# Kernel optimization log

Hardware: AMD Instinct MI355X
Metric: run time of the kernel (lower is better)

## Reference

```python
import jax, jax.numpy as jnp
import numpy as np

N = 50000      # nodes
E = 500000     # edges
D_IN, D_HID, D_OUT = 128, 128, 64


def setup_inputs() -> dict:
    key = jax.random.key(0)
    ks = jax.random.split(key, 9)
    x = jax.random.normal(ks[0], (N, D_IN), dtype=jnp.float32)
    edge_index = jax.random.randint(ks[1], (2, E), 0, N, dtype=jnp.int64)
    s1 = 1.0 / np.sqrt(D_IN)
    s2 = 1.0 / np.sqrt(D_HID)
    W1 = jax.random.normal(ks[2], (D_IN, D_HID), dtype=jnp.float32) * s1
    b1 = jnp.zeros((D_HID,), dtype=jnp.float32)
    W2 = jax.random.normal(ks[3], (D_HID, D_HID), dtype=jnp.float32) * s2
    b2 = jnp.zeros((D_HID,), dtype=jnp.float32)
    W3 = jax.random.normal(ks[4], (D_HID, D_OUT), dtype=jnp.float32) * s2
    b3 = jnp.zeros((D_OUT,), dtype=jnp.float32)
    return {"x": x, "edge_index": edge_index,
            "W1": W1, "b1": b1, "W2": W2, "b2": b2, "W3": W3, "b3": b3}


def _gcn_norm(edge_index, num_nodes):
    # PyG GCNConv default: add self loops, symmetric normalization.
    loop = jnp.arange(num_nodes, dtype=edge_index.dtype)
    src = jnp.concatenate([edge_index[0], loop])  # [E+N]
    dst = jnp.concatenate([edge_index[1], loop])
    deg = jax.ops.segment_sum(jnp.ones_like(dst, dtype=jnp.float32), dst,
                              num_segments=num_nodes)
    dinv = jnp.where(deg > 0, jax.lax.rsqrt(deg), 0.0)
    norm = dinv[src] * dinv[dst]  # [E+N]
    return src, dst, norm


def _gcn_conv(x, W, b, src, dst, norm, num_nodes):
    # linear transform then degree-normalized scatter-add aggregation
    h = x @ W                                 # [N, F_out]
    msg = h[src] * norm[:, None]              # gather + scale  [E+N, F_out]
    out = jax.ops.segment_sum(msg, dst, num_segments=num_nodes)
    return out + b


def reference(x, edge_index, W1, b1, W2, b2, W3, b3):
    src, dst, norm = _gcn_norm(edge_index, N)
    h = _gcn_conv(x, W1, b1, src, dst, norm, N)
    h = _gcn_conv(h, W2, b2, src, dst, norm, N)
    h = _gcn_conv(h, W3, b3, src, dst, norm, N)
    return h
```

## Files before the change

kernel.cpp:

```cpp
#include <hip/hip_runtime.h>

#define DIN 128
#define DHID 128
#define DOUT 64

__device__ __forceinline__ ushort f2bf(float f) {
  unsigned u = __float_as_uint(f);
  return (ushort)((u + 0x7fffu + ((u >> 16) & 1u)) >> 16);
}
__device__ __forceinline__ uint ld_l2(const uint* p) {
  return __hip_atomic_load(p, __ATOMIC_RELAXED, __HIP_MEMORY_SCOPE_AGENT);
}
__device__ __forceinline__ float ld_l2f(const float* p) {
  return __hip_atomic_load(p, __ATOMIC_RELAXED, __HIP_MEMORY_SCOPE_AGENT);
}


__global__ void k_init(int* counts, int* cursor, int n) {
  int i = blockIdx.x * blockDim.x + threadIdx.x;
  if (i < n) { counts[i] = 0; cursor[i] = 0; }
}

__global__ void k_hist(const int* __restrict__ ei, int E, int* __restrict__ counts) {
  int e = blockIdx.x * blockDim.x + threadIdx.x;
  if (e < E) atomicAdd(&counts[__builtin_nontemporal_load(ei + E + e)], 1);
}

__global__ __launch_bounds__(1024) void k_scan1(const int* __restrict__ counts,
                                                int* __restrict__ rowptr,
                                                int* __restrict__ bsums,
                                                float* __restrict__ dinv, int n) {
  __shared__ int s[1024];
  int tid = threadIdx.x;
  int idx = blockIdx.x * 1024 + tid;
  int v = (idx < n) ? counts[idx] : 0;
  if (idx < n) dinv[idx] = 1.0f / sqrtf((float)(v + 1));
  s[tid] = v;
  __syncthreads();
  for (int off = 1; off < 1024; off <<= 1) {
    int t = (tid >= off) ? s[tid - off] : 0;
    __syncthreads();
    s[tid] += t;
    __syncthreads();
  }
  if (idx < n) rowptr[idx] = s[tid] - v;
  if (tid == 1023) bsums[blockIdx.x] = s[1023];
}

__global__ void k_scan2(int* bsums, int nb) {
  int l = threadIdx.x;
  if (nb <= 64) {
    int v = (l < nb) ? bsums[l] : 0;
    int orig = v;
    for (int off = 1; off < 64; off <<= 1) {
      int t = __shfl_up(v, off);
      if (l >= off) v += t;
    }
    if (l < nb) bsums[l] = v - orig;
  } else if (l == 0) {
    int run = 0;
    for (int b = 0; b < nb; ++b) { int v = bsums[b]; bsums[b] = run; run += v; }
  }
}

__global__ __launch_bounds__(1024) void k_scan3(int* __restrict__ rowptr,
                                                const int* __restrict__ bsums, int n, int E) {
  int idx = blockIdx.x * 1024 + threadIdx.x;
  if (idx < n) rowptr[idx] += bsums[blockIdx.x];
  if (idx == 0) rowptr[n] = E;
}

__global__ void k_scatter(const int* __restrict__ ei, int E,
                          const int* __restrict__ rowptr, int* __restrict__ cursor,
                          ushort* __restrict__ csrc) {
  int e = blockIdx.x * blockDim.x + threadIdx.x;
  if (e >= E) return;
  int s = __builtin_nontemporal_load(ei + e);
  int d = __builtin_nontemporal_load(ei + E + e);
  int pos = rowptr[d] + atomicAdd(&cursor[d], 1);
  csrc[pos] = (ushort)s;
}


template <int NCOL>
__global__ void k_mmnaive(const float* __restrict__ A, const float* __restrict__ B,
                          float* __restrict__ C) {
  int t = blockIdx.x * blockDim.x + threadIdx.x;
  if (t >= 128 * NCOL) return;
  int i = t / NCOL, j = t % NCOL;
  float s = 0.f;
  for (int k = 0; k < 128; ++k) s = fmaf(A[i * 128 + k], B[k * NCOL + j], s);
  C[t] = s;
}

__global__ void k_cvec(const float* __restrict__ b1, const float* __restrict__ b2,
                       const float* __restrict__ b3, const float* __restrict__ W2,
                       const float* __restrict__ W3, float* __restrict__ c1,
                       float* __restrict__ c2, float* __restrict__ c3) {
  __shared__ float t1[DHID];
  int j = threadIdx.x;
  float s = 0.f;
  for (int k = 0; k < DHID; ++k) s = fmaf(b1[k], W2[k * DHID + j], s);
  t1[j] = s;
  __syncthreads();
  if (j < DOUT) {
    float a = 0.f, b = 0.f;
    for (int k = 0; k < DHID; ++k) {
      a = fmaf(t1[k], W3[k * DOUT + j], a);
      b = fmaf(b2[k], W3[k * DOUT + j], b);
    }
    c1[j] = a; c2[j] = b; c3[j] = b3[j];
  }
}


__global__ __launch_bounds__(256) void k_xw(const float* __restrict__ X,
                                            const float* __restrict__ Wc,
                                            const float* __restrict__ dinv,
                                            ushort* __restrict__ H, int n) {
  __shared__ float Xs[64][68];
  __shared__ float Ws[64][64];
  int t = threadIdx.x;
  int br = blockIdx.x * 64;
  int r4 = t >> 4, c4 = t & 15;
  float4 acc[4];
#pragma unroll
  for (int i = 0; i < 4; ++i) acc[i] = make_float4(0.f, 0.f, 0.f, 0.f);

  for (int chunk = 0; chunk < 2; ++chunk) {
    int k0 = chunk * 64;
    __syncthreads();
#pragma unroll
    for (int j = 0; j < 4; ++j) {
      int f4 = t + j * 256;
      int row = f4 >> 4, col4 = f4 & 15;
      int gr = br + row;
      float4 v = make_float4(0.f, 0.f, 0.f, 0.f);
      if (gr < n) v = *(const float4*)&X[(size_t)gr * DIN + k0 + col4 * 4];
      *(float4*)&Xs[row][col4 * 4] = v;
      float4 w = *(const float4*)&Wc[(size_t)(k0 + row) * DOUT + col4 * 4];
      *(float4*)&Ws[row][col4 * 4] = w;
    }
    __syncthreads();
#pragma unroll
    for (int kk = 0; kk < 16; ++kk) {
      float4 xv[4], wv[4];
#pragma unroll
      for (int i = 0; i < 4; ++i) xv[i] = *(const float4*)&Xs[r4 * 4 + i][kk * 4];
#pragma unroll
      for (int q = 0; q < 4; ++q) wv[q] = *(const float4*)&Ws[kk * 4 + q][c4 * 4];
#pragma unroll
      for (int i = 0; i < 4; ++i) {
        acc[i].x = fmaf(xv[i].x, wv[0].x, acc[i].x);
        acc[i].y = fmaf(xv[i].x, wv[0].y, acc[i].y);
        acc[i].z = fmaf(xv[i].x, wv[0].z, acc[i].z);
        acc[i].w = fmaf(xv[i].x, wv[0].w, acc[i].w);
        acc[i].x = fmaf(xv[i].y, wv[1].x, acc[i].x);
        acc[i].y = fmaf(xv[i].y, wv[1].y, acc[i].y);
        acc[i].z = fmaf(xv[i].y, wv[1].z, acc[i].z);
        acc[i].w = fmaf(xv[i].y, wv[1].w, acc[i].w);
        acc[i].x = fmaf(xv[i].z, wv[2].x, acc[i].x);
        acc[i].y = fmaf(xv[i].z, wv[2].y, acc[i].y);
        acc[i].z = fmaf(xv[i].z, wv[2].z, acc[i].z);
        acc[i].w = fmaf(xv[i].z, wv[2].w, acc[i].w);
        acc[i].x = fmaf(xv[i].w, wv[3].x, acc[i].x);
        acc[i].y = fmaf(xv[i].w, wv[3].y, acc[i].y);
        acc[i].z = fmaf(xv[i].w, wv[3].z, acc[i].z);
        acc[i].w = fmaf(xv[i].w, wv[3].w, acc[i].w);
      }
    }
  }
#pragma unroll
  for (int i = 0; i < 4; ++i) {
    int gr = br + r4 * 4 + i;
    if (gr < n) {
      float dv = dinv[gr];
      ushort4 hv;
      hv.x = f2bf(acc[i].x * dv); hv.y = f2bf(acc[i].y * dv);
      hv.z = f2bf(acc[i].z * dv); hv.w = f2bf(acc[i].w * dv);
      *(ushort4*)&H[(size_t)gr * DOUT + c4 * 4] = hv;
    }
  }
}


template <int ROUND>
__global__ __launch_bounds__(256) void k_agg(const uint* __restrict__ in,
                                             uint* __restrict__ out16,
                                             float* __restrict__ out32,
                                             const int* __restrict__ rowptr,
                                             const ushort* __restrict__ csrc,
                                             const float* __restrict__ dinv,
                                             float* __restrict__ r1t, float* __restrict__ r1s,
                                             float* __restrict__ r2t,
                                             const float* __restrict__ c1,
                                             const float* __restrict__ c2,
                                             const float* __restrict__ c3, int n) {
  int node = (blockIdx.x * blockDim.x + threadIdx.x) >> 6;
  if (node >= n) return;
  int lane = threadIdx.x & 63;
  int half = lane >> 5;
  int fl   = lane & 31;
  int beg = rowptr[node], end = rowptr[node + 1];
  float di = dinv[node];
  float ax0 = 0.f, ay0 = 0.f, ax1 = 0.f, ay1 = 0.f;
  float ax2 = 0.f, ay2 = 0.f, ax3 = 0.f, ay3 = 0.f;
  float racc = 0.f;
  int e = beg + half;
  for (; e + 6 < end; e += 8) {
    int s0 = csrc[e];
    int s1 = csrc[e + 2];
    int s2 = csrc[e + 4];
    int s3 = csrc[e + 6];
    uint u0 = ld_l2(&in[(size_t)s0 * 32 + fl]);
    uint u1 = ld_l2(&in[(size_t)s1 * 32 + fl]);
    uint u2 = ld_l2(&in[(size_t)s2 * 32 + fl]);
    uint u3 = ld_l2(&in[(size_t)s3 * 32 + fl]);
    ax0 += __uint_as_float(u0 << 16); ay0 += __uint_as_float(u0 & 0xffff0000u);
    ax1 += __uint_as_float(u1 << 16); ay1 += __uint_as_float(u1 & 0xffff0000u);
    ax2 += __uint_as_float(u2 << 16); ay2 += __uint_as_float(u2 & 0xffff0000u);
    ax3 += __uint_as_float(u3 << 16); ay3 += __uint_as_float(u3 & 0xffff0000u);
    if (ROUND == 1) racc += (ld_l2f(&dinv[s0]) + ld_l2f(&dinv[s1]))
                          + (ld_l2f(&dinv[s2]) + ld_l2f(&dinv[s3]));
    if (ROUND == 2) racc += (ld_l2f(&r1s[s0]) + ld_l2f(&r1s[s1]))
                          + (ld_l2f(&r1s[s2]) + ld_l2f(&r1s[s3]));
  }
  for (; e < end; e += 2) {
    int s = csrc[e];
    uint u = ld_l2(&in[(size_t)s * 32 + fl]);
    ax0 += __uint_as_float(u << 16); ay0 += __uint_as_float(u & 0xffff0000u);
    if (ROUND == 1) racc += ld_l2f(&dinv[s]);
    if (ROUND == 2) racc += ld_l2f(&r1s[s]);
  }
  float ax = (ax0 + ax1) + (ax2 + ax3);
  float ay = (ay0 + ay1) + (ay2 + ay3);
  ax += __shfl_xor(ax, 32);
  ay += __shfl_xor(ay, 32);
  if (ROUND != 3) racc += __shfl_xor(racc, 32);
  uint us = in[(size_t)node * 32 + fl];
  float Tx = ax + __uint_as_float(us << 16);
  float Ty = ay + __uint_as_float(us & 0xffff0000u);
  float d2 = di * di;
  if (ROUND == 1) {
    racc += di;
    if (lane == 0) { r1t[node] = di * racc; r1s[node] = d2 * racc; }
  }
  if (ROUND == 2) {
    racc += r1s[node];
    if (lane == 0) r2t[node] = di * racc;
  }
  if (half == 0) {
    if (ROUND == 3) {
      int cf = 2 * fl;
      float vx = fmaf(r1t[node], c2[cf], c3[cf]);
      vx = fmaf(r2t[node], c1[cf], vx);
      float vy = fmaf(r1t[node], c2[cf + 1], c3[cf + 1]);
      vy = fmaf(r2t[node], c1[cf + 1], vy);
      float2 o;
      o.x = fmaf(di, Tx, vx);
      o.y = fmaf(di, Ty, vy);
      *(float2*)&out32[(size_t)node * DOUT + cf] = o;
    } else {
      uint pk = (uint)f2bf(d2 * Tx) | ((uint)f2bf(d2 * Ty) << 16);
      out16[(size_t)node * 32 + fl] = pk;
    }
  }
}


extern "C" void kernel_launch(void* const* d_in, const int* in_sizes, int n_in,
                              void* d_out, int out_size, void* d_ws, size_t ws_size,
                              hipStream_t stream) {
  const float* X  = (const float*)d_in[0];
  const int*   ei = (const int*)d_in[1];
  const float* W1 = (const float*)d_in[2];
  const float* b1 = (const float*)d_in[3];
  const float* W2 = (const float*)d_in[4];
  const float* b2 = (const float*)d_in[5];
  const float* W3 = (const float*)d_in[6];
  const float* b3 = (const float*)d_in[7];
  const int N = in_sizes[0] / DIN;
  const int E = in_sizes[1] / 2;
  float* out = (float*)d_out;

  auto AL = [](size_t x) -> size_t { return (x + 255) & ~(size_t)255; };

  char* p = (char*)d_ws;
  auto alloc = [&](size_t nbytes) -> void* {
    void* r = (void*)p;
    p += AL(nbytes);
    return r;
  };
  int*    rowptr = (int*)alloc((size_t)(N + 1) * 4);
  int*    bsums  = (int*)alloc(256 * 4);
  float*  dinv   = (float*)alloc((size_t)N * 4);
  ushort* csrc   = (ushort*)alloc((size_t)E * 2);
  int*    counts = (int*)alloc((size_t)N * 4);
  int*    cursor = (int*)alloc((size_t)N * 4);
  float*  r2t    = (float*)alloc((size_t)N * 4);
  float*  wtmp   = (float*)alloc((size_t)DIN * DHID * 4);
  float*  wc     = (float*)alloc((size_t)DIN * DOUT * 4);
  float*  c1     = (float*)alloc(DOUT * 4);
  float*  c2     = (float*)alloc(DOUT * 4);
  float*  c3     = (float*)alloc(DOUT * 4);
  uint*   H1     = (uint*)alloc((size_t)N * 32 * 4);
  uint*   H2     = (uint*)alloc((size_t)N * 32 * 4);
  float*  r1t    = (float*)counts;
  float*  r1s    = (float*)cursor;

  k_init<<<(N + 255) / 256, 256, 0, stream>>>(counts, cursor, N);
  k_hist<<<(E + 255) / 256, 256, 0, stream>>>(ei, E, counts);
  int nb = (N + 1023) / 1024;
  k_scan1<<<nb, 1024, 0, stream>>>(counts, rowptr, bsums, dinv, N);
  k_scan2<<<1, 64, 0, stream>>>(bsums, nb);
  k_scan3<<<nb, 1024, 0, stream>>>(rowptr, bsums, N, E);
  k_scatter<<<(E + 255) / 256, 256, 0, stream>>>(ei, E, rowptr, cursor, csrc);

  k_mmnaive<128><<<(128 * 128 + 255) / 256, 256, 0, stream>>>(W1, W2, wtmp);
  k_mmnaive<64><<<(128 * 64 + 255) / 256, 256, 0, stream>>>(wtmp, W3, wc);
  k_cvec<<<1, 128, 0, stream>>>(b1, b2, b3, W2, W3, c1, c2, c3);

  k_xw<<<(N + 63) / 64, 256, 0, stream>>>(X, wc, dinv, (ushort*)H1, N);

  int gb = (N + 3) / 4;
  k_agg<1><<<gb, 256, 0, stream>>>(H1, H2, nullptr, rowptr, csrc, dinv,
                                   r1t, r1s, r2t, c1, c2, c3, N);
  k_agg<2><<<gb, 256, 0, stream>>>(H2, H1, nullptr, rowptr, csrc, dinv,
                                   r1t, r1s, r2t, c1, c2, c3, N);
  k_agg<3><<<gb, 256, 0, stream>>>(H1, nullptr, out, rowptr, csrc, dinv,
                                   r1t, r1s, r2t, c1, c2, c3, N);
}
```

Measured before the change: 180.8 us.

## Merge setup kernels, vectorize edge loads, and enlarge aggregation blocks

Folds the second scan stage into the third (each block redoes the small prefix over the block sums) and seeds the scatter cursor with the final row offsets, so scatter no longer reads rowptr. The W1·W2 product and the bias-vector kernel become one launch, and the init kernel clears only counts, with int4 stores. Histogram and scatter read two edges per thread through int2 loads. Aggregation blocks grow from 256 to 512 threads, and the self-row load is hoisted ahead of the edge loop. Together these cut launch count and small-kernel overhead, though the int2 path depends on E being even.

```diff
diff --git a/kernel.cpp b/kernel.cpp
--- a/kernel.cpp
+++ b/kernel.cpp
@@ -16,14 +16,22 @@
 }
 
 
-__global__ void k_init(int* counts, int* cursor, int n) {
+__global__ void k_init(int* counts, int n4) {
   int i = blockIdx.x * blockDim.x + threadIdx.x;
-  if (i < n) { counts[i] = 0; cursor[i] = 0; }
-}
-
-__global__ void k_hist(const int* __restrict__ ei, int E, int* __restrict__ counts) {
+  if (i < n4) ((int4*)counts)[i] = make_int4(0, 0, 0, 0);
+}
+
+__global__ void k_hist2(const int* __restrict__ ei, int E, int* __restrict__ counts) {
+  int e = (blockIdx.x * blockDim.x + threadIdx.x) * 2;
+  if (e >= E) return;
+  int2 d2 = *(const int2*)&ei[E + e];
+  atomicAdd(&counts[d2.x], 1);
+  if (e + 1 < E) atomicAdd(&counts[d2.y], 1);
+}
+
+__global__ void k_hist1(const int* __restrict__ ei, int E, int* __restrict__ counts) {
   int e = blockIdx.x * blockDim.x + threadIdx.x;
-  if (e < E) atomicAdd(&counts[__builtin_nontemporal_load(ei + E + e)], 1);
+  if (e < E) atomicAdd(&counts[ei[E + e]], 1);
 }
 
 __global__ __launch_bounds__(1024) void k_scan1(const int* __restrict__ counts,
@@ -47,70 +55,96 @@
   if (tid == 1023) bsums[blockIdx.x] = s[1023];
 }
 
-__global__ void k_scan2(int* bsums, int nb) {
-  int l = threadIdx.x;
-  if (nb <= 64) {
-    int v = (l < nb) ? bsums[l] : 0;
+__global__ __launch_bounds__(1024) void k_scan3(int* __restrict__ rowptr,
+                                                const int* __restrict__ bsums,
+                                                int* __restrict__ cursor,
+                                                int n, int E, int nb) {
+  __shared__ int soff;
+  int tid = threadIdx.x;
+  if (tid < 64) {
+    int v = (tid < nb) ? bsums[tid] : 0;
     int orig = v;
     for (int off = 1; off < 64; off <<= 1) {
       int t = __shfl_up(v, off);
-      if (l >= off) v += t;
-    }
-    if (l < nb) bsums[l] = v - orig;
-  } else if (l == 0) {
-    int run = 0;
-    for (int b = 0; b < nb; ++b) { int v = bsums[b]; bsums[b] = run; run += v; }
-  }
-}
-
-__global__ __launch_bounds__(1024) void k_scan3(int* __restrict__ rowptr,
-                                                const int* __restrict__ bsums, int n, int E) {
-  int idx = blockIdx.x * 1024 + threadIdx.x;
-  if (idx < n) rowptr[idx] += bsums[blockIdx.x];
+      if (tid >= off) v += t;
+    }
+    if (tid == blockIdx.x) soff = v - orig;
+  }
+  __syncthreads();
+  int idx = blockIdx.x * 1024 + tid;
+  if (idx < n) {
+    int r = rowptr[idx] + soff;
+    rowptr[idx] = r;
+    cursor[idx] = r;
+  }
   if (idx == 0) rowptr[n] = E;
 }
 
-__global__ void k_scatter(const int* __restrict__ ei, int E,
-                          const int* __restrict__ rowptr, int* __restrict__ cursor,
-                          ushort* __restrict__ csrc) {
+__global__ void k_scatter2(const int* __restrict__ ei, int E,
+                           int* __restrict__ cursor, ushort* __restrict__ csrc) {
+  int e = (blockIdx.x * blockDim.x + threadIdx.x) * 2;
+  if (e >= E) return;
+  int2 s2 = *(const int2*)&ei[e];
+  int2 d2 = *(const int2*)&ei[E + e];
+  int p0 = atomicAdd(&cursor[d2.x], 1);
+  csrc[p0] = (ushort)s2.x;
+  if (e + 1 < E) {
+    int p1 = atomicAdd(&cursor[d2.y], 1);
+    csrc[p1] = (ushort)s2.y;
+  }
+}
+
+__global__ void k_scatter1(const int* __restrict__ ei, int E,
+                           int* __restrict__ cursor, ushort* __restrict__ csrc) {
   int e = blockIdx.x * blockDim.x + threadIdx.x;
   if (e >= E) return;
-  int s = __builtin_nontemporal_load(ei + e);
-  int d = __builtin_nontemporal_load(ei + E + e);
-  int pos = rowptr[d] + atomicAdd(&cursor[d], 1);
+  int s = ei[e];
+  int d = ei[E + e];
+  int pos = atomicAdd(&cursor[d], 1);
   csrc[pos] = (ushort)s;
 }
 
 
-template <int NCOL>
-__global__ void k_mmnaive(const float* __restrict__ A, const float* __restrict__ B,
-                          float* __restrict__ C) {
+__global__ void k_mm1(const float* __restrict__ W1, const float* __restrict__ W2,
+                      float* __restrict__ wtmp,
+                      const float* __restrict__ b1, const float* __restrict__ b2,
+                      const float* __restrict__ b3, const float* __restrict__ W3,
+                      float* __restrict__ c1, float* __restrict__ c2,
+                      float* __restrict__ c3) {
+  if (blockIdx.x < 64) {
+    int t = blockIdx.x * 256 + threadIdx.x;
+    int i = t >> 7, j = t & 127;
+    float s = 0.f;
+    for (int k = 0; k < 128; ++k) s = fmaf(W1[i * 128 + k], W2[k * 128 + j], s);
+    wtmp[t] = s;
+  } else {
+    __shared__ float t1[DHID];
+    int j = threadIdx.x;
+    if (j < DHID) {
+      float s = 0.f;
+      for (int k = 0; k < DHID; ++k) s = fmaf(b1[k], W2[k * DHID + j], s);
+      t1[j] = s;
+    }
+    __syncthreads();
+    if (j < DOUT) {
+      float a = 0.f, b = 0.f;
+      for (int k = 0; k < DHID; ++k) {
+        a = fmaf(t1[k], W3[k * DOUT + j], a);
+        b = fmaf(b2[k], W3[k * DOUT + j], b);
+      }
+      c1[j] = a; c2[j] = b; c3[j] = b3[j];
+    }
+  }
+}
+
+__global__ void k_mm2(const float* __restrict__ A, const float* __restrict__ B,
+                      float* __restrict__ C) {
   int t = blockIdx.x * blockDim.x + threadIdx.x;
-  if (t >= 128 * NCOL) return;
-  int i = t / NCOL, j = t % NCOL;
+  if (t >= 128 * 64) return;
+  int i = t >> 6, j = t & 63;
   float s = 0.f;
-  for (int k = 0; k < 128; ++k) s = fmaf(A[i * 128 + k], B[k * NCOL + j], s);
+  for (int k = 0; k < 128; ++k) s = fmaf(A[i * 128 + k], B[k * 64 + j], s);
   C[t] = s;
-}
-
-__global__ void k_cvec(const float* __restrict__ b1, const float* __restrict__ b2,
-                       const float* __restrict__ b3, const float* __restrict__ W2,
-                       const float* __restrict__ W3, float* __restrict__ c1,
-                       float* __restrict__ c2, float* __restrict__ c3) {
-  __shared__ float t1[DHID];
-  int j = threadIdx.x;
-  float s = 0.f;
-  for (int k = 0; k < DHID; ++k) s = fmaf(b1[k], W2[k * DHID + j], s);
-  t1[j] = s;
-  __syncthreads();
-  if (j < DOUT) {
-    float a = 0.f, b = 0.f;
-    for (int k = 0; k < DHID; ++k) {
-      a = fmaf(t1[k], W3[k * DOUT + j], a);
-      b = fmaf(b2[k], W3[k * DOUT + j], b);
-    }
-    c1[j] = a; c2[j] = b; c3[j] = b3[j];
-  }
 }
 
 
@@ -185,7 +219,7 @@
 
 
 template <int ROUND>
-__global__ __launch_bounds__(256) void k_agg(const uint* __restrict__ in,
+__global__ __launch_bounds__(512) void k_agg(const uint* __restrict__ in,
                                              uint* __restrict__ out16,
                                              float* __restrict__ out32,
                                              const int* __restrict__ rowptr,
@@ -202,6 +236,7 @@
   int half = lane >> 5;
   int fl   = lane & 31;
   int beg = rowptr[node], end = rowptr[node + 1];
+  uint us = in[(size_t)node * 32 + fl];
   float di = dinv[node];
   float ax0 = 0.f, ay0 = 0.f, ax1 = 0.f, ay1 = 0.f;
   float ax2 = 0.f, ay2 = 0.f, ax3 = 0.f, ay3 = 0.f;
@@ -237,7 +272,6 @@
   ax += __shfl_xor(ax, 32);
   ay += __shfl_xor(ay, 32);
   if (ROUND != 3) racc += __shfl_xor(racc, 32);
-  uint us = in[(size_t)node * 32 + fl];
   float Tx = ax + __uint_as_float(us << 16);
   float Ty = ay + __uint_as_float(us & 0xffff0000u);
   float d2 = di * di;
@@ -295,7 +329,7 @@
   int*    bsums  = (int*)alloc(256 * 4);
   float*  dinv   = (float*)alloc((size_t)N * 4);
   ushort* csrc   = (ushort*)alloc((size_t)E * 2);
-  int*    counts = (int*)alloc((size_t)N * 4);
+  int*    counts = (int*)alloc((size_t)(N + 4) * 4);
   int*    cursor = (int*)alloc((size_t)N * 4);
   float*  r2t    = (float*)alloc((size_t)N * 4);
   float*  wtmp   = (float*)alloc((size_t)DIN * DHID * 4);
@@ -308,25 +342,30 @@
   float*  r1t    = (float*)counts;
   float*  r1s    = (float*)cursor;
 
-  k_init<<<(N + 255) / 256, 256, 0, stream>>>(counts, cursor, N);
-  k_hist<<<(E + 255) / 256, 256, 0, stream>>>(ei, E, counts);
+  int n4 = (N + 3) / 4;
+  k_init<<<(n4 + 255) / 256, 256, 0, stream>>>(counts, n4);
+  if ((E & 1) == 0)
+    k_hist2<<<(E / 2 + 255) / 256, 256, 0, stream>>>(ei, E, counts);
+  else
+    k_hist1<<<(E + 255) / 256, 256, 0, stream>>>(ei, E, counts);
   int nb = (N + 1023) / 1024;
   k_scan1<<<nb, 1024, 0, stream>>>(counts, rowptr, bsums, dinv, N);
-  k_scan2<<<1, 64, 0, stream>>>(bsums, nb);
-  k_scan3<<<nb, 1024, 0, stream>>>(rowptr, bsums, N, E);
-  k_scatter<<<(E + 255) / 256, 256, 0, stream>>>(ei, E, rowptr, cursor, csrc);
-
-  k_mmnaive<128><<<(128 * 128 + 255) / 256, 256, 0, stream>>>(W1, W2, wtmp);
-  k_mmnaive<64><<<(128 * 64 + 255) / 256, 256, 0, stream>>>(wtmp, W3, wc);
-  k_cvec<<<1, 128, 0, stream>>>(b1, b2, b3, W2, W3, c1, c2, c3);
+  k_scan3<<<nb, 1024, 0, stream>>>(rowptr, bsums, cursor, N, E, nb);
+  if ((E & 1) == 0)
+    k_scatter2<<<(E / 2 + 255) / 256, 256, 0, stream>>>(ei, E, cursor, csrc);
+  else
+    k_scatter1<<<(E + 255) / 256, 256, 0, stream>>>(ei, E, cursor, csrc);
+
+  k_mm1<<<65, 256, 0, stream>>>(W1, W2, wtmp, b1, b2, b3, W3, c1, c2, c3);
+  k_mm2<<<(128 * 64 + 255) / 256, 256, 0, stream>>>(wtmp, W3, wc);
 
   k_xw<<<(N + 63) / 64, 256, 0, stream>>>(X, wc, dinv, (ushort*)H1, N);
 
-  int gb = (N + 3) / 4;
-  k_agg<1><<<gb, 256, 0, stream>>>(H1, H2, nullptr, rowptr, csrc, dinv,
+  int gb = (N + 7) / 8;
+  k_agg<1><<<gb, 512, 0, stream>>>(H1, H2, nullptr, rowptr, csrc, dinv,
                                    r1t, r1s, r2t, c1, c2, c3, N);
-  k_agg<2><<<gb, 256, 0, stream>>>(H2, H1, nullptr, rowptr, csrc, dinv,
+  k_agg<2><<<gb, 512, 0, stream>>>(H2, H1, nullptr, rowptr, csrc, dinv,
                                    r1t, r1s, r2t, c1, c2, c3, N);
-  k_agg<3><<<gb, 256, 0, stream>>>(H1, nullptr, out, rowptr, csrc, dinv,
+  k_agg<3><<<gb, 512, 0, stream>>>(H1, nullptr, out, rowptr, csrc, dinv,
                                    r1t, r1s, r2t, c1, c2, c3, N);
 }
```

New measurement: 174.1 us. 3.7% less time.
